# Optimization experiments

Hardware: AMD Instinct MI355X
Metric: run time of the kernel (lower is better)

The kernel has to match this reference:

```python
import jax, jax.numpy as jnp
import numpy as np

D_MODEL = 1024
N_HEADS = 16
D_H = D_MODEL // N_HEADS
MAX_LEN = 2048
BATCH = 2
SEQ = 2048
EPS = 1e-8
W_SCALE = 0.02


def _rms_norm(x, w):
    # RMSNorm: x * rsqrt(mean(x^2) + eps) * w
    ms = jnp.mean(jnp.square(x), axis=-1, keepdims=True)
    return w * (x * jax.lax.rsqrt(ms + EPS))


def setup_inputs() -> dict:
    key = jax.random.key(0)
    ks = jax.random.split(key, 12)
    d = D_MODEL
    inp = {
        "x": jax.random.normal(ks[0], (BATCH, SEQ, d), dtype=jnp.float32),
        "t_bias": jnp.zeros((1,), dtype=jnp.float32),  # unused by the module
        "p_bias": jax.random.normal(ks[1], (MAX_LEN, N_HEADS), dtype=jnp.float32),
        # AMS layer params (Linear stored as [in, out])
        "wq": jax.random.normal(ks[2], (d, d), dtype=jnp.float32) * W_SCALE,
        "bq": jnp.zeros((d,), dtype=jnp.float32),
        "wk": jax.random.normal(ks[3], (d, d), dtype=jnp.float32) * W_SCALE,
        "bk": jnp.zeros((d,), dtype=jnp.float32),
        "wv": jax.random.normal(ks[4], (d, d), dtype=jnp.float32) * W_SCALE,
        "bv": jnp.zeros((d,), dtype=jnp.float32),
        "wu": jax.random.normal(ks[5], (d, d), dtype=jnp.float32) * W_SCALE,
        "bu": jnp.zeros((d,), dtype=jnp.float32),
        "g_ams": jnp.ones((d,), dtype=jnp.float32),   # shared RMSNorm weight in AMSLayer
        # MFFN layer params
        "w0": jax.random.normal(ks[6], (d, d), dtype=jnp.float32) * W_SCALE,
        "b0": jnp.zeros((d,), dtype=jnp.float32),
        "w1": jax.random.normal(ks[7], (d, 2 * d), dtype=jnp.float32) * W_SCALE,
        "b1": jnp.zeros((2 * d,), dtype=jnp.float32),
        "w2": jax.random.normal(ks[8], (d, d), dtype=jnp.float32) * W_SCALE,
        "b2": jnp.zeros((d,), dtype=jnp.float32),
        "g_mffn": jnp.ones((d,), dtype=jnp.float32),
    }
    return inp


def reference(x, t_bias, p_bias, wq, bq, wk, bk, wv, bv, wu, bu, g_ams,
              w0, b0, w1, b1, w2, b2, g_mffn):
    B, S, d = x.shape
    H, dh = N_HEADS, D_H

    # ---- AMS layer ----
    x_norm = _rms_norm(x, g_ams)

    def proj(w, b):
        # [B,S,d] -> [B,H,S,dh]
        return (x_norm @ w + b).reshape(B, S, H, dh).transpose(0, 2, 1, 3)

    q = proj(wq, bq)
    k = proj(wk, bk)
    v = proj(wv, bv)

    scale = 1.0 / np.sqrt(dh).astype(np.float32)
    score = jnp.einsum('bhsd,bhtd->bhst', q, k) * scale
    # additive positional bias: p_bias[:S].T -> [H,S], broadcast over query dim
    score = score + p_bias[:S, :].T[None, :, None, :]

    attn = jax.nn.silu(score)                        # SiLU instead of softmax
    out = jnp.einsum('bhst,bhtd->bhsd', attn, v)
    out = out.transpose(0, 2, 1, 3).reshape(B, S, d)

    u = jax.nn.silu(x_norm @ wu + bu)
    ams_out = _rms_norm(out, g_ams) * u

    # ---- MFFN layer ----
    o = (ams_out @ w0 + b0) + x
    o_norm = _rms_norm(o, g_mffn)
    x12 = o_norm @ w1 + b1
    x1, x2 = jnp.split(x12, 2, axis=-1)
    swiglu = jax.nn.silu(x1) * x2
    return (swiglu @ w2 + b2) + o
```

## Files before the change

kernel.cpp:

```cpp
#include <hip/hip_runtime.h>
#include <stdint.h>
#include <math.h>


#define D    1024
#define NH   16
#define DH   64
#define B_   2
#define S_   2048
#define ROWS 4096
#define LQ   4096
#define EPSR 1e-8f

typedef unsigned short u16;
typedef __attribute__((ext_vector_type(8))) short short8;
typedef __attribute__((ext_vector_type(4))) float f32x4;
typedef __attribute__((ext_vector_type(16))) float f32x16;
typedef __attribute__((ext_vector_type(4))) int int4v;

__device__ __forceinline__ float bf2f(u16 u) {
    union { uint32_t i; float f; } c; c.i = ((uint32_t)u) << 16; return c.f;
}
__device__ __forceinline__ u16 f2bf(float f) {
    union { float f; uint32_t i; } c; c.f = f;
    uint32_t x = c.i;
    x += 0x7fffu + ((x >> 16) & 1u);
    return (u16)(x >> 16);
}
#define LOG2E 1.44269504f
__device__ __forceinline__ float silu_fast(float v) {
    return v * __builtin_amdgcn_rcpf(1.0f + __builtin_amdgcn_exp2f(v * -LOG2E));
}

#define GLDS16(gp, lp) __builtin_amdgcn_global_load_lds( \
        (const __attribute__((address_space(1))) void*)(gp), \
        (__attribute__((address_space(3))) void*)(lp), 16, 0, 0)

__device__ __forceinline__ int xcd_work(int flat, int nwg) {
    return ((flat & 7) * (nwg >> 3)) + (flat >> 3);
}

__global__ __launch_bounds__(256) void transpose_all_kernel(
    const float* __restrict__ wq, const float* __restrict__ wk,
    const float* __restrict__ wv, const float* __restrict__ wu,
    const float* __restrict__ w0, const float* __restrict__ w2,
    const float* __restrict__ w1,
    u16* __restrict__ wT4, u16* __restrict__ w0T,
    u16* __restrict__ w2T, u16* __restrict__ w1T,
    const float* __restrict__ pb, float* __restrict__ pbT)
{
    const unsigned MI = 1u << 20;
    const int z = blockIdx.z;
    const int tid = threadIdx.x;
    if (z == 8) {
        if (blockIdx.y != 0) return;
        const int r = (blockIdx.x << 7) + (tid >> 1);
        const int c0 = (tid & 1) << 3;
        float4 v0 = *(const float4*)&pb[(size_t)r * NH + c0];
        float4 v1 = *(const float4*)&pb[(size_t)r * NH + c0 + 4];
        pbT[(size_t)(c0 + 0) * S_ + r] = v0.x;
        pbT[(size_t)(c0 + 1) * S_ + r] = v0.y;
        pbT[(size_t)(c0 + 2) * S_ + r] = v0.z;
        pbT[(size_t)(c0 + 3) * S_ + r] = v0.w;
        pbT[(size_t)(c0 + 4) * S_ + r] = v1.x;
        pbT[(size_t)(c0 + 5) * S_ + r] = v1.y;
        pbT[(size_t)(c0 + 6) * S_ + r] = v1.z;
        pbT[(size_t)(c0 + 7) * S_ + r] = v1.w;
        return;
    }
    const float* W; u16* WT; int N; int noff = 0;
    switch (z) {
        case 0: W = wq; WT = wT4;          N = 1024; break;
        case 1: W = wk; WT = wT4 + 1 * MI; N = 1024; break;
        case 2: W = wv; WT = wT4 + 2 * MI; N = 1024; break;
        case 3: W = wu; WT = wT4 + 3 * MI; N = 1024; break;
        case 4: W = w0; WT = w0T;          N = 1024; break;
        case 5: W = w2; WT = w2T;          N = 1024; break;
        case 6: W = w1; WT = w1T;          N = 2048; noff = 0;    break;
        default:W = w1; WT = w1T;          N = 2048; noff = 1024; break;
    }
    __shared__ float T[64][65];
    const int n0 = (blockIdx.x << 6) + noff;
    const int k0 = blockIdx.y << 6;
    const int rr = tid >> 4;
    const int cc = (tid & 15) << 2;
#pragma unroll
    for (int l = 0; l < 4; ++l) {
        const int r = rr + (l << 4);
        float4 v = *(const float4*)&W[(size_t)(k0 + r) * N + n0 + cc];
        T[cc + 0][r] = v.x; T[cc + 1][r] = v.y;
        T[cc + 2][r] = v.z; T[cc + 3][r] = v.w;
    }
    __syncthreads();
    const int n  = tid >> 2;
    const int ks = (tid & 3) << 4;
#pragma unroll
    for (int m = 0; m < 4; ++m) {
        const int k = ks + (m << 2);
        float4 v = *(const float4*)&T[n][k];
        ushort4 o;
        o.x = f2bf(v.x); o.y = f2bf(v.y); o.z = f2bf(v.z); o.w = f2bf(v.w);
        *(ushort4*)&WT[(size_t)(n0 + n) * 1024 + k0 + k] = o;
    }
}

__global__ __launch_bounds__(256) void rmsnorm_kernel(
    const float* __restrict__ inf, const u16* __restrict__ inb, int ldi,
    const float* __restrict__ g,
    const u16* __restrict__ mul, int ldm,
    u16* __restrict__ out, int ldo)
{
    const int row = blockIdx.x;
    const int tid = threadIdx.x;
    const int c = tid << 2;
    float x0, x1, x2, x3;
    if (inb) {
        ushort4 xi = *(const ushort4*)&inb[(size_t)row * ldi + c];
        x0 = bf2f(xi.x); x1 = bf2f(xi.y); x2 = bf2f(xi.z); x3 = bf2f(xi.w);
    } else {
        float4 xi = *(const float4*)&inf[(size_t)row * ldi + c];
        x0 = xi.x; x1 = xi.y; x2 = xi.z; x3 = xi.w;
    }
    float ss = x0*x0 + x1*x1 + x2*x2 + x3*x3;
#pragma unroll
    for (int off = 32; off > 0; off >>= 1) ss += __shfl_down(ss, off, 64);
    __shared__ float red[4];
    if ((tid & 63) == 0) red[tid >> 6] = ss;
    __syncthreads();
    float r = rsqrtf((red[0] + red[1] + red[2] + red[3]) * (1.0f / D) + EPSR);
    float4 gv = *(const float4*)&g[c];
    float v0 = x0 * r * gv.x, v1 = x1 * r * gv.y, v2 = x2 * r * gv.z, v3 = x3 * r * gv.w;
    if (mul) {
        ushort4 mi = *(const ushort4*)&mul[(size_t)row * ldm + c];
        v0 *= bf2f(mi.x); v1 *= bf2f(mi.y); v2 *= bf2f(mi.z); v3 *= bf2f(mi.w);
    }
    ushort4 o;
    o.x = f2bf(v0); o.y = f2bf(v1); o.z = f2bf(v2); o.w = f2bf(v3);
    *(ushort4*)&out[(size_t)row * ldo + c] = o;
}

__global__ __launch_bounds__(256) void gemm128(
    const u16* __restrict__ A, const u16* __restrict__ WT,
    const float* __restrict__ bs0, const float* __restrict__ bs1,
    const float* __restrict__ bs2, const float* __restrict__ bs3,
    u16* __restrict__ outb, int ldo, int actmask,
    u16* __restrict__ VT, int vtsel)
{
    __shared__ u16 As[128 * 64];
    __shared__ u16 Bs[128 * 64];
    const int tid  = threadIdx.x;
    const int wave = tid >> 6;
    const int lane = tid & 63;
    const int lm   = lane & 15;
    const int quad = lane >> 4;
    const int l7   = lm & 7;
    const int gx   = gridDim.x;
    const int gxm  = gx - 1;
    const int gxs  = __popc(gxm);
    const int work = xcd_work(blockIdx.x + (blockIdx.y << gxs), gx * gridDim.y);
    const int col0 = (work & gxm) << 7;
    const int row0 = (work >> gxs) << 7;
    const int wr = (wave >> 1) << 6;
    const int wc = (wave & 1) << 6;

    const int lr8  = lane >> 3;
    const int gch8 = ((lane & 7) ^ lr8) << 3;
    const u16* Ag = A  + (size_t)(row0 + wave * 32 + lr8) * 1024 + gch8;
    const u16* Bg = WT + (size_t)(col0 + wave * 32 + lr8) * 1024 + gch8;

    f32x4 acc[4][4] = {};

    for (int k0 = 0; k0 < 1024; k0 += 64) {
        __syncthreads();
#pragma unroll
        for (int j = 0; j < 4; ++j) {
            GLDS16(Ag + (size_t)(8 * j) * 1024 + k0, &As[(wave * 32 + 8 * j) * 64]);
            GLDS16(Bg + (size_t)(8 * j) * 1024 + k0, &Bs[(wave * 32 + 8 * j) * 64]);
        }
        __syncthreads();
#pragma unroll
        for (int kk = 0; kk < 2; ++kk) {
            short8 af[4], bf[4];
#pragma unroll
            for (int i = 0; i < 4; ++i)
                af[i] = *(const short8*)&As[(wr + i * 16 + lm) * 64 +
                                            (((kk * 4 + quad) ^ l7) << 3)];
#pragma unroll
            for (int j = 0; j < 4; ++j)
                bf[j] = *(const short8*)&Bs[(wc + j * 16 + lm) * 64 +
                                            (((kk * 4 + quad) ^ l7) << 3)];
#pragma unroll
            for (int i = 0; i < 4; ++i)
#pragma unroll
                for (int j = 0; j < 4; ++j)
                    acc[i][j] = __builtin_amdgcn_mfma_f32_16x16x32_bf16(af[i], bf[j], acc[i][j], 0, 0, 0);
        }
    }
    const int sel = col0 >> 10;
    const float* bias = (sel == 0) ? bs0 : (sel == 1) ? bs1 : (sel == 2) ? bs2 : bs3;
    const int act = (actmask >> sel) & 1;
    if (VT && sel == vtsel) {
        const int b = row0 >> 11;
#pragma unroll
        for (int j = 0; j < 4; ++j) {
            const int c2 = (col0 + wc + j * 16 + lm) & 1023;
            const int h  = c2 >> 6;
            const int dh = c2 & 63;
            const float bj = bias[c2];
            u16* vrow = VT + ((size_t)(b * NH + h) * 64 + dh) * (size_t)S_;
#pragma unroll
            for (int i = 0; i < 4; ++i) {
                const int tb = (row0 & 2047) + wr + i * 16 + quad * 4;
                ushort4 o;
                o.x = f2bf(acc[i][j][0] + bj);
                o.y = f2bf(acc[i][j][1] + bj);
                o.z = f2bf(acc[i][j][2] + bj);
                o.w = f2bf(acc[i][j][3] + bj);
                *(ushort4*)&vrow[tb] = o;
            }
        }
    } else {
#pragma unroll
        for (int j = 0; j < 4; ++j) {
            const int colg = col0 + wc + j * 16 + lm;
            const float bj = bias[colg & 1023];
#pragma unroll
            for (int i = 0; i < 4; ++i) {
#pragma unroll
                for (int r = 0; r < 4; ++r) {
                    const int rowg = row0 + wr + i * 16 + quad * 4 + r;
                    float v = acc[i][j][r] + bj;
                    if (act) v = silu_fast(v);
                    outb[(size_t)rowg * ldo + colg] = f2bf(v);
                }
            }
        }
    }
}

__global__ __launch_bounds__(256) void gemm64(
    const u16* __restrict__ A, int lda, const u16* __restrict__ WT,
    const float* __restrict__ bias,
    const float* __restrict__ res,
    float* __restrict__ outf, int ldo)
{
    __shared__ u16 As[128 * 64];
    __shared__ u16 Bs[64 * 64];
    const int tid  = threadIdx.x;
    const int wave = tid >> 6;
    const int lane = tid & 63;
    const int lm   = lane & 15;
    const int quad = lane >> 4;
    const int l7   = lm & 7;
    const int gx   = gridDim.x;
    const int gxm  = gx - 1;
    const int gxs  = __popc(gxm);
    const int work = xcd_work(blockIdx.x + (blockIdx.y << gxs), gx * gridDim.y);
    const int col0 = (work & gxm) << 6;
    const int row0 = (work >> gxs) << 7;
    const int wr = (wave >> 1) << 6;
    const int wc = (wave & 1) << 5;

    const int lr8  = lane >> 3;
    const int gch8 = ((lane & 7) ^ lr8) << 3;
    const u16* Ag = A  + (size_t)(row0 + wave * 32 + lr8) * lda + gch8;
    const u16* Bg = WT + (size_t)(col0 + wave * 16 + lr8) * 1024 + gch8;

    f32x4 acc[4][2] = {};

    for (int k0 = 0; k0 < 1024; k0 += 64) {
        __syncthreads();
#pragma unroll
        for (int j = 0; j < 4; ++j)
            GLDS16(Ag + (size_t)(8 * j) * lda + k0, &As[(wave * 32 + 8 * j) * 64]);
#pragma unroll
        for (int j = 0; j < 2; ++j)
            GLDS16(Bg + (size_t)(8 * j) * 1024 + k0, &Bs[(wave * 16 + 8 * j) * 64]);
        __syncthreads();
#pragma unroll
        for (int kk = 0; kk < 2; ++kk) {
            short8 af[4], bf[2];
#pragma unroll
            for (int i = 0; i < 4; ++i)
                af[i] = *(const short8*)&As[(wr + i * 16 + lm) * 64 +
                                            (((kk * 4 + quad) ^ l7) << 3)];
#pragma unroll
            for (int j = 0; j < 2; ++j)
                bf[j] = *(const short8*)&Bs[(wc + j * 16 + lm) * 64 +
                                            (((kk * 4 + quad) ^ l7) << 3)];
#pragma unroll
            for (int i = 0; i < 4; ++i)
#pragma unroll
                for (int j = 0; j < 2; ++j)
                    acc[i][j] = __builtin_amdgcn_mfma_f32_16x16x32_bf16(af[i], bf[j], acc[i][j], 0, 0, 0);
        }
    }
#pragma unroll
    for (int j = 0; j < 2; ++j) {
        const int colg = col0 + wc + j * 16 + lm;
        const float bj = bias[colg];
#pragma unroll
        for (int i = 0; i < 4; ++i) {
#pragma unroll
            for (int r = 0; r < 4; ++r) {
                const int rowg = row0 + wr + i * 16 + quad * 4 + r;
                const size_t idx = (size_t)rowg * ldo + colg;
                float v = acc[i][j][r] + bj;
                if (res) v += res[idx];
                outf[idx] = v;
            }
        }
    }
}

__global__ __launch_bounds__(256) void gemm_w1_swiglu(
    const u16* __restrict__ A, const u16* __restrict__ WT,
    const float* __restrict__ b1, u16* __restrict__ outb)
{
    __shared__ u16 As[128 * 64];
    __shared__ u16 Bs[128 * 64];
    const int tid  = threadIdx.x;
    const int wave = tid >> 6;
    const int lane = tid & 63;
    const int lm   = lane & 15;
    const int quad = lane >> 4;
    const int l7   = lm & 7;
    const int gx   = gridDim.x;
    const int gxm  = gx - 1;
    const int gxs  = __popc(gxm);
    const int work = xcd_work(blockIdx.x + (blockIdx.y << gxs), gx * gridDim.y);
    const int col0 = (work & gxm) << 6;
    const int row0 = (work >> gxs) << 7;
    const int wr  = (wave >> 1) << 6;
    const int wc2 = (wave & 1) << 5;

    const int lr8  = lane >> 3;
    const int gch8 = ((lane & 7) ^ lr8) << 3;
    const int sb   = wave * 32;
    const int brow = col0 + (sb & 63) + ((sb >> 6) << 10) + lr8;
    const u16* Ag = A  + (size_t)(row0 + wave * 32 + lr8) * 1024 + gch8;
    const u16* Bg = WT + (size_t)brow * 1024 + gch8;

    f32x4 acc[4][4] = {};

    for (int k0 = 0; k0 < 1024; k0 += 64) {
        __syncthreads();
#pragma unroll
        for (int j = 0; j < 4; ++j) {
            GLDS16(Ag + (size_t)(8 * j) * 1024 + k0, &As[(wave * 32 + 8 * j) * 64]);
            GLDS16(Bg + (size_t)(8 * j) * 1024 + k0, &Bs[(wave * 32 + 8 * j) * 64]);
        }
        __syncthreads();
#pragma unroll
        for (int kk = 0; kk < 2; ++kk) {
            short8 af[4], bf[4];
#pragma unroll
            for (int i = 0; i < 4; ++i)
                af[i] = *(const short8*)&As[(wr + i * 16 + lm) * 64 +
                                            (((kk * 4 + quad) ^ l7) << 3)];
#pragma unroll
            for (int j = 0; j < 2; ++j) {
                bf[j]     = *(const short8*)&Bs[(wc2 + j * 16 + lm) * 64 +
                                                (((kk * 4 + quad) ^ l7) << 3)];
                bf[j + 2] = *(const short8*)&Bs[(64 + wc2 + j * 16 + lm) * 64 +
                                                (((kk * 4 + quad) ^ l7) << 3)];
            }
#pragma unroll
            for (int i = 0; i < 4; ++i)
#pragma unroll
                for (int j = 0; j < 4; ++j)
                    acc[i][j] = __builtin_amdgcn_mfma_f32_16x16x32_bf16(af[i], bf[j], acc[i][j], 0, 0, 0);
        }
    }
#pragma unroll
    for (int j = 0; j < 2; ++j) {
        const int colg = col0 + wc2 + j * 16 + lm;
        const float ba = b1[colg];
        const float bb = b1[1024 + colg];
#pragma unroll
        for (int i = 0; i < 4; ++i) {
#pragma unroll
            for (int r = 0; r < 4; ++r) {
                const int rowg = row0 + wr + i * 16 + quad * 4 + r;
                const float x1v = acc[i][j][r] + ba;
                const float x2v = acc[i][j + 2][r] + bb;
                outb[(size_t)rowg * LQ + colg] = f2bf(silu_fast(x1v) * x2v);
            }
        }
    }
}

__global__ __launch_bounds__(512, 2) void attn_mfma(
    const u16* __restrict__ qkvu, const u16* __restrict__ VT,
    const float* __restrict__ pbT, u16* __restrict__ out)
{
    __shared__ u16 Ks[2][2][64 * 64];
    __shared__ u16 Vs[2][2][64 * 64];
    __shared__ float pbl[S_];
    const int tid  = threadIdx.x;
    const int wave = tid >> 6;
    const int grp  = wave >> 2;
    const int wq4  = wave & 3;
    const int lane = tid & 63;
    const int l31  = lane & 31;
    const int hi   = lane >> 5;
    const int l7   = lane & 7;
    const int xorv = l7 ^ ((l31 >> 3) & 3);
    const int flat = blockIdx.x + (blockIdx.y << 4) + (blockIdx.z << 8);
    const int work = ((flat & 7) << 6) + (flat >> 3);
    const int s0 = (work & 15) << 7;
    const int h  = (work >> 4) & 15;
    const int b  = work >> 8;
    const size_t base = (size_t)b * S_ * LQ + (size_t)h * DH;
    const u16* q  = qkvu + base;
    const u16* kg = qkvu + base + 1024;
    const u16* vt = VT + (size_t)(b * NH + h) * 64 * S_;
    const float* pbh = pbT + (size_t)h * S_;

    for (int i = tid * 4; i < S_; i += 2048)
        *(float4*)&pbl[i] = *(const float4*)&pbh[i];

    const int qrow = s0 + wq4 * 32 + l31;
    short8 qf[4];
#pragma unroll
    for (int i = 0; i < 4; ++i)
        qf[i] = *(const short8*)&q[(size_t)qrow * LQ + i * 16 + hi * 8];

    const int lr  = lane >> 3;
    const int gA  = (2 * wq4) & 3;
    const int gB  = (2 * wq4 + 1) & 3;
    const u16* kgA = kg + (size_t)(16 * wq4 + lr) * LQ     + ((l7 ^ lr ^ gA) << 3);
    const u16* kgB = kg + (size_t)(16 * wq4 + 8 + lr) * LQ + ((l7 ^ lr ^ gB) << 3);
    const u16* vgA = vt + (size_t)(16 * wq4 + lr) * S_     + ((l7 ^ lr ^ gA) << 3);
    const u16* vgB = vt + (size_t)(16 * wq4 + 8 + lr) * S_ + ((l7 ^ lr ^ gB) << 3);

#define ISSUE(it, bu) do { \
        const size_t tn = ((size_t)(grp) * 16 + (size_t)(it)) << 6; \
        GLDS16(kgA + tn * LQ, &Ks[grp][bu][(16 * wq4) * 64]); \
        GLDS16(kgB + tn * LQ, &Ks[grp][bu][(16 * wq4 + 8) * 64]); \
        GLDS16(vgA + tn,      &Vs[grp][bu][(16 * wq4) * 64]); \
        GLDS16(vgB + tn,      &Vs[grp][bu][(16 * wq4 + 8) * 64]); \
    } while (0)

    f32x16 accO[2] = {};
    ISSUE(0, 0);
    __syncthreads();

#pragma unroll 1
    for (int it = 0; it < 16; ++it) {
        const int ib = it & 1;
        const int nb = ib ^ 1;
        if (it + 1 < 16) ISSUE(it + 1, nb);
        const int t0 = grp * 1024 + (it << 6);
        f32x16 st0 = {}, st1 = {};
        __builtin_amdgcn_s_setprio(1);
#pragma unroll
        for (int i = 0; i < 4; ++i) {
            const int co = ((2 * i + hi) ^ xorv) << 3;
            short8 kf0 = *(const short8*)&Ks[grp][ib][(l31) * 64 + co];
            short8 kf1 = *(const short8*)&Ks[grp][ib][(32 + l31) * 64 + co];
            st0 = __builtin_amdgcn_mfma_f32_32x32x16_bf16(kf0, qf[i], st0, 0, 0, 0);
            st1 = __builtin_amdgcn_mfma_f32_32x32x16_bf16(kf1, qf[i], st1, 0, 0, 0);
        }
        __builtin_amdgcn_s_setprio(0);
        int pk0[8], pk1[8];
#pragma unroll
        for (int g = 0; g < 4; ++g) {
            float4 pbv0 = *(const float4*)&pbl[t0 + 8 * g + 4 * hi];
            float4 pbv1 = *(const float4*)&pbl[t0 + 32 + 8 * g + 4 * hi];
            float a0 = silu_fast(fmaf(st0[4 * g + 0], 0.125f, pbv0.x));
            float a1 = silu_fast(fmaf(st0[4 * g + 1], 0.125f, pbv0.y));
            float a2 = silu_fast(fmaf(st0[4 * g + 2], 0.125f, pbv0.z));
            float a3 = silu_fast(fmaf(st0[4 * g + 3], 0.125f, pbv0.w));
            float b0 = silu_fast(fmaf(st1[4 * g + 0], 0.125f, pbv1.x));
            float b1 = silu_fast(fmaf(st1[4 * g + 1], 0.125f, pbv1.y));
            float b2 = silu_fast(fmaf(st1[4 * g + 2], 0.125f, pbv1.z));
            float b3 = silu_fast(fmaf(st1[4 * g + 3], 0.125f, pbv1.w));
            asm("v_cvt_pk_bf16_f32 %0, %1, %2" : "=v"(pk0[2 * g])     : "v"(a0), "v"(a1));
            asm("v_cvt_pk_bf16_f32 %0, %1, %2" : "=v"(pk0[2 * g + 1]) : "v"(a2), "v"(a3));
            asm("v_cvt_pk_bf16_f32 %0, %1, %2" : "=v"(pk1[2 * g])     : "v"(b0), "v"(b1));
            asm("v_cvt_pk_bf16_f32 %0, %1, %2" : "=v"(pk1[2 * g + 1]) : "v"(b2), "v"(b3));
        }
#pragma unroll
        for (int m = 0; m < 2; ++m) {
            int w0 = pk0[4 * m + 0], w2 = pk0[4 * m + 2];
            int w1 = pk0[4 * m + 1], w3 = pk0[4 * m + 3];
            asm("v_permlane32_swap_b32 %0, %1" : "+v"(w0), "+v"(w2));
            asm("v_permlane32_swap_b32 %0, %1" : "+v"(w1), "+v"(w3));
            int u0 = pk1[4 * m + 0], u2 = pk1[4 * m + 2];
            int u1 = pk1[4 * m + 1], u3 = pk1[4 * m + 3];
            asm("v_permlane32_swap_b32 %0, %1" : "+v"(u0), "+v"(u2));
            asm("v_permlane32_swap_b32 %0, %1" : "+v"(u1), "+v"(u3));
            union { int4v i; short8 s; } pa, pb2;
            pa.i.x  = w0; pa.i.y  = w1; pa.i.z  = w2; pa.i.w  = w3;
            pb2.i.x = u0; pb2.i.y = u1; pb2.i.z = u2; pb2.i.w = u3;
            __builtin_amdgcn_s_setprio(1);
#pragma unroll
            for (int n = 0; n < 2; ++n) {
                short8 vf0 = *(const short8*)&Vs[grp][ib][(32 * n + l31) * 64 +
                    (((2 * m + hi) ^ xorv) << 3)];
                short8 vf1 = *(const short8*)&Vs[grp][ib][(32 * n + l31) * 64 +
                    (((4 + 2 * m + hi) ^ xorv) << 3)];
                accO[n] = __builtin_amdgcn_mfma_f32_32x32x16_bf16(pa.s,  vf0, accO[n], 0, 0, 0);
                accO[n] = __builtin_amdgcn_mfma_f32_32x32x16_bf16(pb2.s, vf1, accO[n], 0, 0, 0);
            }
            __builtin_amdgcn_s_setprio(0);
        }
        __syncthreads();
    }
#undef ISSUE
    float* scr = (float*)&Ks[0][0][0];
    const int sl = wq4 * 64 + lane;
    if (grp == 1) {
#pragma unroll
        for (int n = 0; n < 2; ++n)
#pragma unroll
            for (int r = 0; r < 16; ++r)
                scr[(n * 16 + r) * 256 + sl] = accO[n][r];
    }
    __syncthreads();
    if (grp == 0) {
#pragma unroll
        for (int n = 0; n < 2; ++n)
#pragma unroll
            for (int r = 0; r < 16; ++r)
                accO[n][r] += scr[(n * 16 + r) * 256 + sl];
        const int qb = s0 + wq4 * 32 + 4 * hi;
#pragma unroll
        for (int n = 0; n < 2; ++n)
#pragma unroll
            for (int r = 0; r < 16; ++r) {
                const int qq = qb + (r & 3) + 8 * (r >> 2);
                out[base + (size_t)qq * LQ + 32 * n + l31] = f2bf(accO[n][r]);
            }
    }
}

extern "C" void kernel_launch(void* const* d_in, const int* in_sizes, int n_in,
                              void* d_out, int out_size, void* d_ws, size_t ws_size,
                              hipStream_t stream)
{
    const float* x      = (const float*)d_in[0];
    const float* pb     = (const float*)d_in[2];
    const float* wq     = (const float*)d_in[3];
    const float* bq     = (const float*)d_in[4];
    const float* wk     = (const float*)d_in[5];
    const float* bk     = (const float*)d_in[6];
    const float* wv     = (const float*)d_in[7];
    const float* bv     = (const float*)d_in[8];
    const float* wu     = (const float*)d_in[9];
    const float* bu     = (const float*)d_in[10];
    const float* g_ams  = (const float*)d_in[11];
    const float* w0     = (const float*)d_in[12];
    const float* b0     = (const float*)d_in[13];
    const float* w1     = (const float*)d_in[14];
    const float* b1     = (const float*)d_in[15];
    const float* w2     = (const float*)d_in[16];
    const float* b2     = (const float*)d_in[17];
    const float* g_mffn = (const float*)d_in[18];
    float* OUT = (float*)d_out;
    u16*   VT  = (u16*)d_out;
    float* pbT = (float*)((u16*)d_out + 4 * (1u << 20));

    const size_t MI = 1024 * 1024;
    u16* WS   = (u16*)d_ws;
    u16* wT4  = WS;
    u16* w0T  = WS + 4 * MI;
    u16* w2T  = WS + 5 * MI;
    u16* w1T  = WS + 6 * MI;
    u16* A0   = WS + 8 * MI;
    u16* QKVU = WS + 12 * MI;

    dim3 blk(256);

    transpose_all_kernel<<<dim3(16, 16, 9), blk, 0, stream>>>(
        wq, wk, wv, wu, w0, w2, w1, wT4, w0T, w2T, w1T, pb, pbT);

    rmsnorm_kernel<<<ROWS, blk, 0, stream>>>(x, nullptr, D, g_ams, nullptr, 0, A0, D);
    gemm128<<<dim3(32, 32), blk, 0, stream>>>(A0, wT4, bq, bk, bv, bu,
                                              QKVU, LQ, 0b1000, VT, 2);
    attn_mfma<<<dim3(16, 16, 2), dim3(512), 0, stream>>>(QKVU, VT, pbT, QKVU);
    rmsnorm_kernel<<<ROWS, blk, 0, stream>>>(nullptr, QKVU, LQ, g_ams, QKVU + 3072, LQ, A0, D);
    gemm64<<<dim3(16, 32), blk, 0, stream>>>(A0, D, w0T, b0, x, OUT, D);
    rmsnorm_kernel<<<ROWS, blk, 0, stream>>>(OUT, nullptr, D, g_mffn, nullptr, 0, A0, D);
    gemm_w1_swiglu<<<dim3(16, 32), blk, 0, stream>>>(A0, w1T, b1, QKVU + 2048);
    gemm64<<<dim3(16, 32), blk, 0, stream>>>(QKVU + 2048, LQ, w2T, b2, OUT, OUT, D);
    (void)ws_size; (void)in_sizes; (void)n_in; (void)out_size;
}
```

Before: 297.8 us.

## Double-buffer LDS tiles in GEMM kernels to overlap global loads with MFMA

The three GEMM kernels (gemm128, gemm64, gemm_w1_swiglu) now keep two LDS buffers for A and B. Each iteration issues global-to-LDS loads for the next K tile before running MFMAs on the current one, using explicit vmcnt waits and raw barriers. The aim is to hide global memory latency behind matrix math instead of stalling on every tile. It doubles LDS use per block, which can lower occupancy, and it relies on hand-counted vmcnt values being correct.

After: 299.4 us. No clear change (+0.6%).

```diff
diff --git a/kernel.cpp b/kernel.cpp
--- a/kernel.cpp
+++ b/kernel.cpp
@@ -146,8 +146,8 @@
     u16* __restrict__ outb, int ldo, int actmask,
     u16* __restrict__ VT, int vtsel)
 {
-    __shared__ u16 As[128 * 64];
-    __shared__ u16 Bs[128 * 64];
+    __shared__ u16 As[2][128 * 64];
+    __shared__ u16 Bs[2][128 * 64];
     const int tid  = threadIdx.x;
     const int wave = tid >> 6;
     const int lane = tid & 63;
@@ -168,34 +168,49 @@
     const u16* Ag = A  + (size_t)(row0 + wave * 32 + lr8) * 1024 + gch8;
     const u16* Bg = WT + (size_t)(col0 + wave * 32 + lr8) * 1024 + gch8;
 
+#define G128_ISSUE(bu, k0) do { \
+        u16* Asd = &As[bu][(wave * 32) * 64]; \
+        u16* Bsd = &Bs[bu][(wave * 32) * 64]; \
+        _Pragma("unroll") \
+        for (int j = 0; j < 4; ++j) { \
+            GLDS16(Ag + (size_t)(8 * j) * 1024 + (k0), Asd + (8 * j) * 64); \
+            GLDS16(Bg + (size_t)(8 * j) * 1024 + (k0), Bsd + (8 * j) * 64); \
+        } \
+    } while (0)
+
     f32x4 acc[4][4] = {};
-
-    for (int k0 = 0; k0 < 1024; k0 += 64) {
-        __syncthreads();
-#pragma unroll
-        for (int j = 0; j < 4; ++j) {
-            GLDS16(Ag + (size_t)(8 * j) * 1024 + k0, &As[(wave * 32 + 8 * j) * 64]);
-            GLDS16(Bg + (size_t)(8 * j) * 1024 + k0, &Bs[(wave * 32 + 8 * j) * 64]);
-        }
-        __syncthreads();
+    G128_ISSUE(0, 0);
+
+#pragma unroll 1
+    for (int it = 0; it < 16; ++it) {
+        const int ib = it & 1;
+        const int nb = ib ^ 1;
+        if (it < 15) G128_ISSUE(nb, (it + 1) * 64);
+        if (it < 15) asm volatile("s_waitcnt vmcnt(8)" ::: "memory");
+        else         asm volatile("s_waitcnt vmcnt(0)" ::: "memory");
+        __builtin_amdgcn_s_barrier();
+        asm volatile("" ::: "memory");
 #pragma unroll
         for (int kk = 0; kk < 2; ++kk) {
             short8 af[4], bf[4];
 #pragma unroll
             for (int i = 0; i < 4; ++i)
-                af[i] = *(const short8*)&As[(wr + i * 16 + lm) * 64 +
-                                            (((kk * 4 + quad) ^ l7) << 3)];
+                af[i] = *(const short8*)&As[ib][(wr + i * 16 + lm) * 64 +
+                                               (((kk * 4 + quad) ^ l7) << 3)];
 #pragma unroll
             for (int j = 0; j < 4; ++j)
-                bf[j] = *(const short8*)&Bs[(wc + j * 16 + lm) * 64 +
-                                            (((kk * 4 + quad) ^ l7) << 3)];
+                bf[j] = *(const short8*)&Bs[ib][(wc + j * 16 + lm) * 64 +
+                                               (((kk * 4 + quad) ^ l7) << 3)];
 #pragma unroll
             for (int i = 0; i < 4; ++i)
 #pragma unroll
                 for (int j = 0; j < 4; ++j)
                     acc[i][j] = __builtin_amdgcn_mfma_f32_16x16x32_bf16(af[i], bf[j], acc[i][j], 0, 0, 0);
         }
-    }
+        asm volatile("" ::: "memory");
+        __builtin_amdgcn_s_barrier();
+    }
+#undef G128_ISSUE
     const int sel = col0 >> 10;
     const float* bias = (sel == 0) ? bs0 : (sel == 1) ? bs1 : (sel == 2) ? bs2 : bs3;
     const int act = (actmask >> sel) & 1;
@@ -244,8 +259,8 @@
     const float* __restrict__ res,
     float* __restrict__ outf, int ldo)
 {
-    __shared__ u16 As[128 * 64];
-    __shared__ u16 Bs[64 * 64];
+    __shared__ u16 As[2][128 * 64];
+    __shared__ u16 Bs[2][64 * 64];
     const int tid  = threadIdx.x;
     const int wave = tid >> 6;
     const int lane = tid & 63;
@@ -266,35 +281,50 @@
     const u16* Ag = A  + (size_t)(row0 + wave * 32 + lr8) * lda + gch8;
     const u16* Bg = WT + (size_t)(col0 + wave * 16 + lr8) * 1024 + gch8;
 
+#define G64_ISSUE(bu, k0) do { \
+        u16* Asd = &As[bu][(wave * 32) * 64]; \
+        u16* Bsd = &Bs[bu][(wave * 16) * 64]; \
+        _Pragma("unroll") \
+        for (int j = 0; j < 4; ++j) \
+            GLDS16(Ag + (size_t)(8 * j) * lda + (k0), Asd + (8 * j) * 64); \
+        _Pragma("unroll") \
+        for (int j = 0; j < 2; ++j) \
+            GLDS16(Bg + (size_t)(8 * j) * 1024 + (k0), Bsd + (8 * j) * 64); \
+    } while (0)
+
     f32x4 acc[4][2] = {};
-
-    for (int k0 = 0; k0 < 1024; k0 += 64) {
-        __syncthreads();
-#pragma unroll
-        for (int j = 0; j < 4; ++j)
-            GLDS16(Ag + (size_t)(8 * j) * lda + k0, &As[(wave * 32 + 8 * j) * 64]);
-#pragma unroll
-        for (int j = 0; j < 2; ++j)
-            GLDS16(Bg + (size_t)(8 * j) * 1024 + k0, &Bs[(wave * 16 + 8 * j) * 64]);
-        __syncthreads();
+    G64_ISSUE(0, 0);
+
+#pragma unroll 1
+    for (int it = 0; it < 16; ++it) {
+        const int ib = it & 1;
+        const int nb = ib ^ 1;
+        if (it < 15) G64_ISSUE(nb, (it + 1) * 64);
+        if (it < 15) asm volatile("s_waitcnt vmcnt(6)" ::: "memory");
+        else         asm volatile("s_waitcnt vmcnt(0)" ::: "memory");
+        __builtin_amdgcn_s_barrier();
+        asm volatile("" ::: "memory");
 #pragma unroll
         for (int kk = 0; kk < 2; ++kk) {
             short8 af[4], bf[2];
 #pragma unroll
             for (int i = 0; i < 4; ++i)
-                af[i] = *(const short8*)&As[(wr + i * 16 + lm) * 64 +
-                                            (((kk * 4 + quad) ^ l7) << 3)];
+                af[i] = *(const short8*)&As[ib][(wr + i * 16 + lm) * 64 +
+                                               (((kk * 4 + quad) ^ l7) << 3)];
 #pragma unroll
             for (int j = 0; j < 2; ++j)
-                bf[j] = *(const short8*)&Bs[(wc + j * 16 + lm) * 64 +
-                                            (((kk * 4 + quad) ^ l7) << 3)];
+                bf[j] = *(const short8*)&Bs[ib][(wc + j * 16 + lm) * 64 +
+                                               (((kk * 4 + quad) ^ l7) << 3)];
 #pragma unroll
             for (int i = 0; i < 4; ++i)
 #pragma unroll
                 for (int j = 0; j < 2; ++j)
                     acc[i][j] = __builtin_amdgcn_mfma_f32_16x16x32_bf16(af[i], bf[j], acc[i][j], 0, 0, 0);
         }
-    }
+        asm volatile("" ::: "memory");
+        __builtin_amdgcn_s_barrier();
+    }
+#undef G64_ISSUE
 #pragma unroll
     for (int j = 0; j < 2; ++j) {
         const int colg = col0 + wc + j * 16 + lm;
@@ -317,8 +347,8 @@
     const u16* __restrict__ A, const u16* __restrict__ WT,
     const float* __restrict__ b1, u16* __restrict__ outb)
 {
-    __shared__ u16 As[128 * 64];
-    __shared__ u16 Bs[128 * 64];
+    __shared__ u16 As[2][128 * 64];
+    __shared__ u16 Bs[2][128 * 64];
     const int tid  = threadIdx.x;
     const int wave = tid >> 6;
     const int lane = tid & 63;
@@ -341,29 +371,41 @@
     const u16* Ag = A  + (size_t)(row0 + wave * 32 + lr8) * 1024 + gch8;
     const u16* Bg = WT + (size_t)brow * 1024 + gch8;
 
+#define GW1_ISSUE(bu, k0) do { \
+        u16* Asd = &As[bu][(wave * 32) * 64]; \
+        u16* Bsd = &Bs[bu][(wave * 32) * 64]; \
+        _Pragma("unroll") \
+        for (int j = 0; j < 4; ++j) { \
+            GLDS16(Ag + (size_t)(8 * j) * 1024 + (k0), Asd + (8 * j) * 64); \
+            GLDS16(Bg + (size_t)(8 * j) * 1024 + (k0), Bsd + (8 * j) * 64); \
+        } \
+    } while (0)
+
     f32x4 acc[4][4] = {};
-
-    for (int k0 = 0; k0 < 1024; k0 += 64) {
-        __syncthreads();
-#pragma unroll
-        for (int j = 0; j < 4; ++j) {
-            GLDS16(Ag + (size_t)(8 * j) * 1024 + k0, &As[(wave * 32 + 8 * j) * 64]);
-            GLDS16(Bg + (size_t)(8 * j) * 1024 + k0, &Bs[(wave * 32 + 8 * j) * 64]);
-        }
-        __syncthreads();
+    GW1_ISSUE(0, 0);
+
+#pragma unroll 1
+    for (int it = 0; it < 16; ++it) {
+        const int ib = it & 1;
+        const int nb = ib ^ 1;
+        if (it < 15) GW1_ISSUE(nb, (it + 1) * 64);
+        if (it < 15) asm volatile("s_waitcnt vmcnt(8)" ::: "memory");
+        else         asm volatile("s_waitcnt vmcnt(0)" ::: "memory");
+        __builtin_amdgcn_s_barrier();
+        asm volatile("" ::: "memory");
 #pragma unroll
         for (int kk = 0; kk < 2; ++kk) {
             short8 af[4], bf[4];
 #pragma unroll
             for (int i = 0; i < 4; ++i)
-                af[i] = *(const short8*)&As[(wr + i * 16 + lm) * 64 +
-                                            (((kk * 4 + quad) ^ l7) << 3)];
+                af[i] = *(const short8*)&As[ib][(wr + i * 16 + lm) * 64 +
+                                               (((kk * 4 + quad) ^ l7) << 3)];
 #pragma unroll
             for (int j = 0; j < 2; ++j) {
-                bf[j]     = *(const short8*)&Bs[(wc2 + j * 16 + lm) * 64 +
-                                                (((kk * 4 + quad) ^ l7) << 3)];
-                bf[j + 2] = *(const short8*)&Bs[(64 + wc2 + j * 16 + lm) * 64 +
-                                                (((kk * 4 + quad) ^ l7) << 3)];
+                bf[j]     = *(const short8*)&Bs[ib][(wc2 + j * 16 + lm) * 64 +
+                                                    (((kk * 4 + quad) ^ l7) << 3)];
+                bf[j + 2] = *(const short8*)&Bs[ib][(64 + wc2 + j * 16 + lm) * 64 +
+                                                    (((kk * 4 + quad) ^ l7) << 3)];
             }
 #pragma unroll
             for (int i = 0; i < 4; ++i)
@@ -371,7 +413,10 @@
                 for (int j = 0; j < 4; ++j)
                     acc[i][j] = __builtin_amdgcn_mfma_f32_16x16x32_bf16(af[i], bf[j], acc[i][j], 0, 0, 0);
         }
-    }
+        asm volatile("" ::: "memory");
+        __builtin_amdgcn_s_barrier();
+    }
+#undef GW1_ISSUE
 #pragma unroll
     for (int j = 0; j < 2; ++j) {
         const int colg = col0 + wc2 + j * 16 + lm;
```

## Replace QKVU GEMM with 256x256 double-buffered 8-wave pipelined kernel

Applied to the files above, without the earlier changes.

Replaces the fused QKV+U projection GEMM, which used 128x128 tiles, 4 waves and single-buffered LDS, with a 256x256-tile, 8-wave kernel. The new kernel double-buffers LDS and interleaves global-to-LDS loads for the next k-slice with MFMA compute in fine-grained barrier phases. It also raises wave priority around the MFMA bursts. The aim is to hide memory latency and raise arithmetic intensity per LDS byte. In exchange it uses far more LDS and registers per block and launches only 256 workgroups, which risks poor occupancy or load balance across CUs.

Result: no change. 302.4 us (+1.5%).

```diff
diff --git a/kernel.cpp b/kernel.cpp
--- a/kernel.cpp
+++ b/kernel.cpp
@@ -139,97 +139,146 @@
     *(ushort4*)&out[(size_t)row * ldo + c] = o;
 }
 
-__global__ __launch_bounds__(256) void gemm128(
+__global__ __launch_bounds__(512, 2) void gemm256(
     const u16* __restrict__ A, const u16* __restrict__ WT,
     const float* __restrict__ bs0, const float* __restrict__ bs1,
     const float* __restrict__ bs2, const float* __restrict__ bs3,
     u16* __restrict__ outb, int ldo, int actmask,
     u16* __restrict__ VT, int vtsel)
 {
-    __shared__ u16 As[128 * 64];
-    __shared__ u16 Bs[128 * 64];
+    __shared__ u16 As[2][256 * 64];
+    __shared__ u16 Bs[2][256 * 64];
     const int tid  = threadIdx.x;
     const int wave = tid >> 6;
     const int lane = tid & 63;
     const int lm   = lane & 15;
     const int quad = lane >> 4;
-    const int l7   = lm & 7;
-    const int gx   = gridDim.x;
-    const int gxm  = gx - 1;
-    const int gxs  = __popc(gxm);
-    const int work = xcd_work(blockIdx.x + (blockIdx.y << gxs), gx * gridDim.y);
-    const int col0 = (work & gxm) << 7;
-    const int row0 = (work >> gxs) << 7;
-    const int wr = (wave >> 1) << 6;
-    const int wc = (wave & 1) << 6;
+    const int l7x  = lm & 7;
+    const int wm   = wave >> 2;
+    const int wn   = wave & 3;
+    const int work = xcd_work(blockIdx.x, 256);
+    const int row0 = (work >> 4) << 8;
+    const int col0 = (work & 15) << 8;
 
     const int lr8  = lane >> 3;
     const int gch8 = ((lane & 7) ^ lr8) << 3;
-    const u16* Ag = A  + (size_t)(row0 + wave * 32 + lr8) * 1024 + gch8;
-    const u16* Bg = WT + (size_t)(col0 + wave * 32 + lr8) * 1024 + gch8;
-
-    f32x4 acc[4][4] = {};
-
-    for (int k0 = 0; k0 < 1024; k0 += 64) {
-        __syncthreads();
-#pragma unroll
-        for (int j = 0; j < 4; ++j) {
-            GLDS16(Ag + (size_t)(8 * j) * 1024 + k0, &As[(wave * 32 + 8 * j) * 64]);
-            GLDS16(Bg + (size_t)(8 * j) * 1024 + k0, &Bs[(wave * 32 + 8 * j) * 64]);
-        }
-        __syncthreads();
-#pragma unroll
-        for (int kk = 0; kk < 2; ++kk) {
-            short8 af[4], bf[4];
-#pragma unroll
-            for (int i = 0; i < 4; ++i)
-                af[i] = *(const short8*)&As[(wr + i * 16 + lm) * 64 +
-                                            (((kk * 4 + quad) ^ l7) << 3)];
-#pragma unroll
-            for (int j = 0; j < 4; ++j)
-                bf[j] = *(const short8*)&Bs[(wc + j * 16 + lm) * 64 +
-                                            (((kk * 4 + quad) ^ l7) << 3)];
-#pragma unroll
-            for (int i = 0; i < 4; ++i)
-#pragma unroll
-                for (int j = 0; j < 4; ++j)
-                    acc[i][j] = __builtin_amdgcn_mfma_f32_16x16x32_bf16(af[i], bf[j], acc[i][j], 0, 0, 0);
-        }
-    }
+    const u16* Ag = A  + (size_t)(row0 + 16 * wave + lr8) * 1024 + gch8;
+    const u16* Bg = WT + (size_t)(col0 + 16 * wave + lr8) * 1024 + gch8;
+
+#define STG(arr, buf, hf, gbase, kofs) do { \
+        u16* dst = &arr[buf][((hf) * 128 + 16 * wave) * 64]; \
+        GLDS16(gbase + (size_t)((hf) * 128) * 1024 + (kofs), dst); \
+        GLDS16(gbase + (size_t)((hf) * 128 + 8) * 1024 + (kofs), dst + 8 * 64); \
+    } while (0)
+#define PH_BARRIER() do { asm volatile("" ::: "memory"); \
+        __builtin_amdgcn_s_barrier(); asm volatile("" ::: "memory"); } while (0)
+#define PH_COMPUTE(buf, q) do { \
+        short8 af[2][2]; \
+        _Pragma("unroll") \
+        for (int ii = 0; ii < 2; ++ii) \
+            _Pragma("unroll") \
+            for (int kk = 0; kk < 2; ++kk) \
+                af[ii][kk] = *(const short8*)&As[buf][(128 * wm + 16 * (2 * (q) + ii) + lm) * 64 + \
+                                                     (((kk * 4 + quad) ^ l7x) << 3)]; \
+        if ((q) == 0) { \
+            _Pragma("unroll") \
+            for (int n = 0; n < 4; ++n) \
+                _Pragma("unroll") \
+                for (int kk = 0; kk < 2; ++kk) \
+                    bf[n][kk] = *(const short8*)&Bs[buf][(64 * wn + 16 * n + lm) * 64 + \
+                                                         (((kk * 4 + quad) ^ l7x) << 3)]; \
+        } \
+        __builtin_amdgcn_s_setprio(1); \
+        _Pragma("unroll") \
+        for (int ii = 0; ii < 2; ++ii) \
+            _Pragma("unroll") \
+            for (int n = 0; n < 4; ++n) \
+                _Pragma("unroll") \
+                for (int kk = 0; kk < 2; ++kk) \
+                    acc[2 * (q) + ii][n] = __builtin_amdgcn_mfma_f32_16x16x32_bf16( \
+                        af[ii][kk], bf[n][kk], acc[2 * (q) + ii][n], 0, 0, 0); \
+        __builtin_amdgcn_s_setprio(0); \
+    } while (0)
+
+    f32x4 acc[8][4] = {};
+    short8 bf[4][2];
+
+    STG(Bs, 0, 0, Bg, 0); STG(Bs, 0, 1, Bg, 0);
+    STG(As, 0, 0, Ag, 0); STG(As, 0, 1, Ag, 0);
+    STG(Bs, 1, 0, Bg, 64); STG(Bs, 1, 1, Bg, 64);
+
+#pragma unroll 1
+    for (int i7 = 0; i7 < 8; ++i7) {
+        const int t1k = (2 * i7 + 1) * 64;
+        const int t2k = t1k + 64;
+        const int t3k = t2k + 64;
+        const bool more = (i7 < 7);
+        asm volatile("s_waitcnt vmcnt(4)" ::: "memory");
+        PH_BARRIER();
+        STG(As, 1, 0, Ag, t1k);
+        PH_COMPUTE(0, 0);
+        PH_BARRIER();
+        STG(As, 1, 1, Ag, t1k);
+        PH_COMPUTE(0, 1);
+        PH_BARRIER();
+        if (more) STG(Bs, 0, 0, Bg, t2k);
+        PH_COMPUTE(0, 2);
+        PH_BARRIER();
+        if (more) STG(Bs, 0, 1, Bg, t2k);
+        PH_COMPUTE(0, 3);
+        if (more) asm volatile("s_waitcnt vmcnt(4)" ::: "memory");
+        else      asm volatile("s_waitcnt vmcnt(0)" ::: "memory");
+        PH_BARRIER();
+        if (more) STG(As, 0, 0, Ag, t2k);
+        PH_COMPUTE(1, 0);
+        PH_BARRIER();
+        if (more) STG(As, 0, 1, Ag, t2k);
+        PH_COMPUTE(1, 1);
+        PH_BARRIER();
+        if (more) STG(Bs, 1, 0, Bg, t3k);
+        PH_COMPUTE(1, 2);
+        PH_BARRIER();
+        if (more) STG(Bs, 1, 1, Bg, t3k);
+        PH_COMPUTE(1, 3);
+    }
+#undef PH_COMPUTE
+#undef PH_BARRIER
+#undef STG
+
     const int sel = col0 >> 10;
     const float* bias = (sel == 0) ? bs0 : (sel == 1) ? bs1 : (sel == 2) ? bs2 : bs3;
     const int act = (actmask >> sel) & 1;
     if (VT && sel == vtsel) {
         const int b = row0 >> 11;
 #pragma unroll
-        for (int j = 0; j < 4; ++j) {
-            const int c2 = (col0 + wc + j * 16 + lm) & 1023;
+        for (int n = 0; n < 4; ++n) {
+            const int c2 = (col0 + 64 * wn + 16 * n + lm) & 1023;
             const int h  = c2 >> 6;
             const int dh = c2 & 63;
             const float bj = bias[c2];
             u16* vrow = VT + ((size_t)(b * NH + h) * 64 + dh) * (size_t)S_;
 #pragma unroll
-            for (int i = 0; i < 4; ++i) {
-                const int tb = (row0 & 2047) + wr + i * 16 + quad * 4;
+            for (int i = 0; i < 8; ++i) {
+                const int tb = (row0 & 2047) + 128 * wm + 16 * i + quad * 4;
                 ushort4 o;
-                o.x = f2bf(acc[i][j][0] + bj);
-                o.y = f2bf(acc[i][j][1] + bj);
-                o.z = f2bf(acc[i][j][2] + bj);
-                o.w = f2bf(acc[i][j][3] + bj);
+                o.x = f2bf(acc[i][n][0] + bj);
+                o.y = f2bf(acc[i][n][1] + bj);
+                o.z = f2bf(acc[i][n][2] + bj);
+                o.w = f2bf(acc[i][n][3] + bj);
                 *(ushort4*)&vrow[tb] = o;
             }
         }
     } else {
 #pragma unroll
-        for (int j = 0; j < 4; ++j) {
-            const int colg = col0 + wc + j * 16 + lm;
+        for (int n = 0; n < 4; ++n) {
+            const int colg = col0 + 64 * wn + 16 * n + lm;
             const float bj = bias[colg & 1023];
 #pragma unroll
-            for (int i = 0; i < 4; ++i) {
+            for (int i = 0; i < 8; ++i) {
 #pragma unroll
                 for (int r = 0; r < 4; ++r) {
-                    const int rowg = row0 + wr + i * 16 + quad * 4 + r;
-                    float v = acc[i][j][r] + bj;
+                    const int rowg = row0 + 128 * wm + 16 * i + quad * 4 + r;
+                    float v = acc[i][n][r] + bj;
                     if (act) v = silu_fast(v);
                     outb[(size_t)rowg * ldo + colg] = f2bf(v);
                 }
@@ -577,8 +626,8 @@
         wq, wk, wv, wu, w0, w2, w1, wT4, w0T, w2T, w1T, pb, pbT);
 
     rmsnorm_kernel<<<ROWS, blk, 0, stream>>>(x, nullptr, D, g_ams, nullptr, 0, A0, D);
-    gemm128<<<dim3(32, 32), blk, 0, stream>>>(A0, wT4, bq, bk, bv, bu,
-                                              QKVU, LQ, 0b1000, VT, 2);
+    gemm256<<<dim3(256), dim3(512), 0, stream>>>(A0, wT4, bq, bk, bv, bu,
+                                                 QKVU, LQ, 0b1000, VT, 2);
     attn_mfma<<<dim3(16, 16, 2), dim3(512), 0, stream>>>(QKVU, VT, pbT, QKVU);
     rmsnorm_kernel<<<ROWS, blk, 0, stream>>>(nullptr, QKVU, LQ, g_ams, QKVU + 3072, LQ, A0, D);
     gemm64<<<dim3(16, 32), blk, 0, stream>>>(A0, D, w0T, b0, x, OUT, D);
```
